# Optimization experiments

Measured on AMD Instinct MI355X. Metric: run time of the kernel, lower is better.

The kernel has to match this reference:

```python
import jax, jax.numpy as jnp
import numpy as np

B, L = 4096, 200
N_USERS, N_ITEMS, N_CATS, N_DUR = 200000, 500000, 1000, 20
D = 64  # item_embed_dim == seq_embed_dim


def _lin(k, din, dout):
    kw, kb = jax.random.split(k)
    s = 1.0 / np.sqrt(din)
    return (jax.random.uniform(kw, (din, dout), minval=-s, maxval=s),
            jax.random.uniform(kb, (dout,), minval=-s, maxval=s))


def setup_inputs() -> dict:
    key = jax.random.key(0)
    ks = jax.random.split(key, 20)
    inp = {
        'user_id': jax.random.randint(ks[0], (B,), 0, N_USERS),
        'item_id': jax.random.randint(ks[1], (B,), 0, N_ITEMS),
        'item_category': jax.random.randint(ks[2], (B,), 0, N_CATS),
        'item_dur_bkt': jax.random.randint(ks[3], (B,), 0, N_DUR),
        'user_dense': jax.random.normal(ks[4], (B, 25), dtype=jnp.float32),
        'item_dense': jax.random.normal(ks[5], (B, 3), dtype=jnp.float32),
        'history_seq': jax.random.randint(ks[6], (B, L), 0, N_ITEMS + 1),
        # embedding tables (init std=0.01 as in _init_weights)
        'user_W': 0.01 * jax.random.normal(ks[7], (N_USERS, 64), dtype=jnp.float32),
        'item_W': 0.01 * jax.random.normal(ks[8], (N_ITEMS, D), dtype=jnp.float32),
        'cat_W': 0.01 * jax.random.normal(ks[9], (N_CATS, 16), dtype=jnp.float32),
        'dur_W': 0.01 * jax.random.normal(ks[10], (N_DUR, 8), dtype=jnp.float32),
        'hist_W': 0.01 * jax.random.normal(ks[11], (N_ITEMS + 1, D), dtype=jnp.float32),
    }
    # attention MLP: 4*D=256 -> 64 -> 32 -> 1
    inp['aW0'], inp['ab0'] = _lin(ks[12], 4 * D, 64)
    inp['aW1'], inp['ab1'] = _lin(ks[13], 64, 32)
    inp['aW2'], inp['ab2'] = _lin(ks[14], 32, 1)
    # final MLP: concat_dim 64+64+16+8+25+3+64 = 244 -> 256 -> 128 -> 1
    inp['mW0'], inp['mb0'] = _lin(ks[15], 244, 256)
    inp['mW1'], inp['mb1'] = _lin(ks[16], 256, 128)
    inp['mW2'], inp['mb2'] = _lin(ks[17], 128, 1)
    return inp


def reference(user_id, item_id, item_category, item_dur_bkt, user_dense, item_dense,
              history_seq, user_W, item_W, cat_W, dur_W, hist_W,
              aW0, ab0, aW1, ab1, aW2, ab2, mW0, mb0, mW1, mb1, mW2, mb2):
    u_emb = user_W[user_id]            # (B, 64)
    i_emb = item_W[item_id]            # (B, D)
    c_emb = cat_W[item_category]       # (B, 16)
    d_emb = dur_W[item_dur_bkt]        # (B, 8)
    hist = hist_W[history_seq]         # (B, L, D)

    t = i_emb[:, None, :]              # (B, 1, D); item_dim == seq_dim so no slice
    tb = jnp.broadcast_to(t, hist.shape)
    feat = jnp.concatenate([hist, tb, hist * t, hist - t], axis=-1)  # (B, L, 4D)

    h = jax.nn.relu(feat @ aW0 + ab0)
    h = jax.nn.relu(h @ aW1 + ab1)
    scores = (h @ aW2 + ab2)[..., 0]   # (B, L)

    pad_mask = history_seq == 0
    scores = jnp.where(pad_mask, jnp.float32(-1e9), scores)
    w = jax.nn.softmax(scores, axis=-1)                # (B, L)
    pooled = jnp.einsum('bl,bld->bd', w, hist)         # (B, D)

    x = jnp.concatenate([u_emb, i_emb, c_emb, d_emb, user_dense, item_dense, pooled], axis=-1)
    h = jax.nn.relu(x @ mW0 + mb0)     # dropout is identity in eval mode
    h = jax.nn.relu(h @ mW1 + mb1)
    logit = (h @ mW2 + mb2)[..., 0]
    return jax.nn.sigmoid(logit)       # (B,)
```

## Files before the change

kernel.cpp:

```cpp
#include <hip/hip_runtime.h>

#define L_SZ 200
#define RB 8
#define HS_STRIDE 72

typedef __attribute__((ext_vector_type(8))) short short8;
typedef __attribute__((ext_vector_type(4))) float floatx4;

__device__ __forceinline__ unsigned short f2bf(float f) {
    unsigned int u = __float_as_uint(f);
    unsigned int r = (u + 0x7fffu + ((u >> 16) & 1u)) >> 16;
    return (unsigned short)r;
}
__device__ __forceinline__ float bf2f(unsigned short h) {
    return __uint_as_float(((unsigned int)h) << 16);
}
__device__ __forceinline__ float wave_sum64(float v) {
    #pragma unroll
    for (int m = 1; m <= 32; m <<= 1) v += __shfl_xor(v, m, 64);
    return v;
}
__device__ __forceinline__ float wave_max64(float v) {
    #pragma unroll
    for (int m = 1; m <= 32; m <<= 1) v = fmaxf(v, __shfl_xor(v, m, 64));
    return v;
}
__device__ __forceinline__ unsigned int pk2(float a, float b) {
    return ((unsigned int)f2bf(b) << 16) | (unsigned int)f2bf(a);
}

__global__ __launch_bounds__(256) void prep_kernel(
    const int* __restrict__ item_id, const float* __restrict__ item_W,
    const float* __restrict__ aW0, const float* __restrict__ ab0,
    const float* __restrict__ aW1,
    float* __restrict__ T1t, float* __restrict__ T2t,
    unsigned short* __restrict__ PW1, float* __restrict__ cb_ws)
{
    __shared__ float shbuf[3 * 64 * 65];
    const int tid = threadIdx.x;
    if (blockIdx.x == 0) {
        #pragma unroll
        for (int t = 0; t < 3; ++t) {
            const int r0 = (t == 0) ? 0 : (t == 1) ? 128 : 192;
            for (int u = tid; u < 1024; u += 256) {
                int k = u >> 4, c4 = u & 15;
                float4 v = *(const float4*)(aW0 + (r0 + k) * 64 + c4 * 4);
                float* dst = shbuf + t * 4160 + k * 65 + c4 * 4;
                dst[0] = v.x; dst[1] = v.y; dst[2] = v.z; dst[3] = v.w;
            }
        }
        __syncthreads();
        for (int u = tid; u < 4096; u += 256) {
            int j = u >> 6, k = u & 63;
            T1t[u] = shbuf[k * 65 + j] + shbuf[2 * 4160 + k * 65 + j];
            T2t[u] = shbuf[4160 + k * 65 + j];
        }
        for (int u = tid; u < 2048; u += 256) {
            int i = u & 7, lane = (u >> 3) & 63, f = u >> 9;
            int nt = f >> 1, ks = f & 1;
            int k = ks * 32 + (lane >> 4) * 8 + i;
            int n = nt * 16 + (lane & 15);
            PW1[u] = f2bf(aW1[k * 32 + n]);
        }
    } else {
        for (int u = tid; u < 4096; u += 256) {
            int k = u >> 6, j = u & 63;
            shbuf[k * 65 + j] = aW0[(64 + k) * 64 + j] - aW0[(192 + k) * 64 + j];
        }
        __syncthreads();
        const int bl = tid >> 6, j = tid & 63;
        const int b = (blockIdx.x - 1) * 4 + bl;
        const float* ie = item_W + (size_t)item_id[b] * 64;
        float acc = ab0[j];
        #pragma unroll 8
        for (int k = 0; k < 64; ++k) acc = fmaf(ie[k], shbuf[k * 65 + j], acc);
        cb_ws[(size_t)b * 64 + j] = acc;
    }
}

__global__ __launch_bounds__(256, 4) void attn_kernel(
    const int* __restrict__ item_id, const int* __restrict__ hist_seq,
    const float* __restrict__ item_W, const float* __restrict__ hist_W,
    const float* __restrict__ T1t, const float* __restrict__ T2t,
    const unsigned short* __restrict__ PW1, const float* __restrict__ cb_ws,
    const float* __restrict__ ab1, const float* __restrict__ aW2,
    const float* __restrict__ ab2, float* __restrict__ pooled_ws)
{
    __shared__ __align__(16) unsigned char smem[38624];
    unsigned short* Hs  = (unsigned short*)(smem);
    unsigned short* BB  = (unsigned short*)(smem + 28800);
    int*   seq_sh = (int*)(smem + 36992);
    float* scores = (float*)(smem + 37792);
    float* red    = (float*)(smem + 38592);

    const int tid  = threadIdx.x;
    const int w    = tid >> 6;
    const int lane = tid & 63;
    const int b    = blockIdx.x;
    const int* hseq = hist_seq + b * L_SZ;

    if (tid < L_SZ) seq_sh[tid] = hseq[tid];

    const int rbase = tid >> 3, c8 = tid & 7;
    const bool extra = tid < 64;
    const int r6 = extra ? 192 + rbase : 0;
    const float* sp[7];
    #pragma unroll
    for (int t = 0; t < 6; ++t)
        sp[t] = hist_W + (size_t)hseq[rbase + t * 32] * 64 + c8 * 8;
    sp[6] = hist_W + (size_t)hseq[r6] * 64 + c8 * 8;
    float4 f0[7], f1[7];
    #pragma unroll
    for (int t = 0; t < 7; ++t) {
        f0[t] = *(const float4*)sp[t];
        f1[t] = *(const float4*)(sp[t] + 4);
    }

    const int c = lane & 15, q = lane >> 4;
    short8 bW1[2][2];
    #pragma unroll
    for (int nt = 0; nt < 2; ++nt)
        #pragma unroll
        for (int ks = 0; ks < 2; ++ks)
            bW1[nt][ks] = *(const short8*)(PW1 + ((nt * 2 + ks) * 64 + lane) * 8);
    float cbr[4];
    #pragma unroll
    for (int nt = 0; nt < 4; ++nt) cbr[nt] = cb_ws[(size_t)b * 64 + nt * 16 + c];
    float ab1r[2], aw2r[2];
    #pragma unroll
    for (int nt = 0; nt < 2; ++nt) {
        ab1r[nt] = ab1[nt * 16 + c];
        aw2r[nt] = aW2[nt * 16 + c];
    }
    const float ab2s = ab2[0];

    #pragma unroll
    for (int t = 0; t < 6; ++t) {
        uint4 pk;
        pk.x = pk2(f0[t].x, f0[t].y); pk.y = pk2(f0[t].z, f0[t].w);
        pk.z = pk2(f1[t].x, f1[t].y); pk.w = pk2(f1[t].z, f1[t].w);
        *(uint4*)(Hs + (rbase + t * 32) * HS_STRIDE + c8 * 8) = pk;
    }
    if (extra) {
        uint4 pk;
        pk.x = pk2(f0[6].x, f0[6].y); pk.y = pk2(f0[6].z, f0[6].w);
        pk.z = pk2(f1[6].x, f1[6].y); pk.w = pk2(f1[6].z, f1[6].w);
        *(uint4*)(Hs + r6 * HS_STRIDE + c8 * 8) = pk;
    }

    {
        const float* irow = item_W + (size_t)item_id[b] * 64;
        const int j0 = tid >> 3;
        float4 em0 = *(const float4*)(irow + c8 * 8);
        float4 em1 = *(const float4*)(irow + c8 * 8 + 4);
        #pragma unroll
        for (int t = 0; t < 2; ++t) {
            int j = j0 + t * 32;
            const float* p1 = T1t + j * 64 + c8 * 8;
            const float* p2 = T2t + j * 64 + c8 * 8;
            float4 a0 = *(const float4*)p1, a1 = *(const float4*)(p1 + 4);
            float4 b0 = *(const float4*)p2, b1 = *(const float4*)(p2 + 4);
            float v[8];
            v[0] = a0.x + em0.x * b0.x; v[1] = a0.y + em0.y * b0.y;
            v[2] = a0.z + em0.z * b0.z; v[3] = a0.w + em0.w * b0.w;
            v[4] = a1.x + em1.x * b1.x; v[5] = a1.y + em1.y * b1.y;
            v[6] = a1.z + em1.z * b1.z; v[7] = a1.w + em1.w * b1.w;
            uint4 pk;
            pk.x = pk2(v[0], v[1]); pk.y = pk2(v[2], v[3]);
            pk.z = pk2(v[4], v[5]); pk.w = pk2(v[6], v[7]);
            *(uint4*)(BB + j * 64 + (c8 ^ (j & 7)) * 8) = pk;
        }
    }
    __syncthreads();

    short8 bW[4][2];
    #pragma unroll
    for (int nt = 0; nt < 4; ++nt)
        #pragma unroll
        for (int ks = 0; ks < 2; ++ks)
            bW[nt][ks] = *(const short8*)(BB + (nt * 16 + c) * 64
                                             + ((4 * ks + q) ^ (c & 7)) * 8);
    __syncthreads();

    unsigned short* scrw = BB + w * (16 * 64);
    const floatx4 zf = {0.f, 0.f, 0.f, 0.f};

    for (int mt = w; mt < 13; mt += 4) {
        const int rowbase = mt * 16;
        floatx4 acc0[4] = {zf, zf, zf, zf};
        #pragma unroll
        for (int ks = 0; ks < 2; ++ks) {
            short8 a = *(const short8*)(Hs + (rowbase + c) * HS_STRIDE + ks * 32 + q * 8);
            acc0[0] = __builtin_amdgcn_mfma_f32_16x16x32_bf16(a, bW[0][ks], acc0[0], 0, 0, 0);
            acc0[1] = __builtin_amdgcn_mfma_f32_16x16x32_bf16(a, bW[1][ks], acc0[1], 0, 0, 0);
            acc0[2] = __builtin_amdgcn_mfma_f32_16x16x32_bf16(a, bW[2][ks], acc0[2], 0, 0, 0);
            acc0[3] = __builtin_amdgcn_mfma_f32_16x16x32_bf16(a, bW[3][ks], acc0[3], 0, 0, 0);
        }
        #pragma unroll
        for (int nt = 0; nt < 4; ++nt)
            #pragma unroll
            for (int r = 0; r < 4; ++r) {
                float h = fmaxf(acc0[nt][r] + cbr[nt], 0.f);
                int row = q * 4 + r;
                int gp = (2 * nt + (c >> 3)) ^ (row & 7);
                scrw[row * 64 + gp * 8 + (c & 7)] = f2bf(h);
            }
        floatx4 acc1[2] = {zf, zf};
        #pragma unroll
        for (int ks = 0; ks < 2; ++ks) {
            short8 a1 = *(const short8*)(scrw + c * 64 + ((4 * ks + q) ^ (c & 7)) * 8);
            acc1[0] = __builtin_amdgcn_mfma_f32_16x16x32_bf16(a1, bW1[0][ks], acc1[0], 0, 0, 0);
            acc1[1] = __builtin_amdgcn_mfma_f32_16x16x32_bf16(a1, bW1[1][ks], acc1[1], 0, 0, 0);
        }
        float s[4];
        #pragma unroll
        for (int r = 0; r < 4; ++r)
            s[r] = fmaxf(acc1[0][r] + ab1r[0], 0.f) * aw2r[0]
                 + fmaxf(acc1[1][r] + ab1r[1], 0.f) * aw2r[1];
        #pragma unroll
        for (int m = 1; m <= 8; m <<= 1)
            #pragma unroll
            for (int r = 0; r < 4; ++r) s[r] += __shfl_xor(s[r], m, 64);
        if (c == 0) {
            #pragma unroll
            for (int r = 0; r < 4; ++r) {
                int l = rowbase + q * 4 + r;
                if (l < L_SZ)
                    scores[l] = (seq_sh[l] == 0) ? -1.0e9f : (s[r] + ab2s);
            }
        }
    }
    __syncthreads();

    float s0 = (tid < L_SZ) ? scores[tid] : -3.0e38f;
    float mx = wave_max64(s0);
    if (lane == 0) red[w] = mx;
    __syncthreads();
    mx = fmaxf(fmaxf(red[0], red[1]), fmaxf(red[2], red[3]));
    float e = (tid < L_SZ) ? __expf(s0 - mx) : 0.f;
    float sm = wave_sum64(e);
    if (lane == 0) red[4 + w] = sm;
    __syncthreads();
    const float winv = 1.f / ((red[4] + red[5]) + (red[6] + red[7]));
    if (tid < L_SZ) scores[tid] = e * winv;
    __syncthreads();

    float* pools = (float*)BB;
    {
        int g  = (w << 1) | (lane >> 5);
        int jj = lane & 31;
        int l0 = g * 26, l1 = (l0 + 26 < L_SZ) ? l0 + 26 : L_SZ;
        float p0 = 0.f, p1 = 0.f;
        for (int l = l0; l < l1; ++l) {
            float wt = scores[l];
            unsigned int pv = *(const unsigned int*)(Hs + l * HS_STRIDE + jj * 2);
            p0 = fmaf(wt, bf2f((unsigned short)(pv & 0xffffu)), p0);
            p1 = fmaf(wt, bf2f((unsigned short)(pv >> 16)), p1);
        }
        float2 pp = {p0, p1};
        *(float2*)&pools[g * 64 + jj * 2] = pp;
    }
    __syncthreads();
    if (tid < 64) {
        float sum = 0.f;
        #pragma unroll
        for (int g = 0; g < 8; ++g) sum += pools[g * 64 + tid];
        pooled_ws[(size_t)b * 64 + tid] = sum;
    }
}

__global__ __launch_bounds__(256) void mlp_kernel(
    const int* __restrict__ user_id, const int* __restrict__ item_id,
    const int* __restrict__ item_cat, const int* __restrict__ item_dur,
    const float* __restrict__ user_dense, const float* __restrict__ item_dense,
    const float* __restrict__ user_W, const float* __restrict__ item_W,
    const float* __restrict__ cat_W, const float* __restrict__ dur_W,
    const float* __restrict__ mW0, const float* __restrict__ mb0,
    const float* __restrict__ mW1, const float* __restrict__ mb1,
    const float* __restrict__ mW2, const float* __restrict__ mb2,
    const float* __restrict__ pooled_ws, float* __restrict__ out)
{
    __shared__ __align__(16) float xT[244][RB];
    __shared__ __align__(16) float h0T[256][RB];
    __shared__ __align__(16) float h1T[128][RB];
    __shared__ __align__(16) float part[128][RB];

    const int tid = threadIdx.x;
    const int b0 = blockIdx.x * RB;

    for (int idx = tid; idx < 244 * RB; idx += 256) {
        int r = idx / 244;
        int c = idx - r * 244;
        int b = b0 + r;
        float v;
        if (c < 64)       v = user_W[(size_t)user_id[b] * 64 + c];
        else if (c < 128) v = item_W[(size_t)item_id[b] * 64 + (c - 64)];
        else if (c < 144) v = cat_W[item_cat[b] * 16 + (c - 128)];
        else if (c < 152) v = dur_W[item_dur[b] * 8 + (c - 144)];
        else if (c < 177) v = user_dense[b * 25 + (c - 152)];
        else if (c < 180) v = item_dense[b * 3 + (c - 177)];
        else              v = pooled_ws[(size_t)b * 64 + (c - 180)];
        xT[c][r] = v;
    }
    __syncthreads();

    {
        float acc[RB];
        const float bias = mb0[tid];
        #pragma unroll
        for (int r = 0; r < RB; ++r) acc[r] = bias;
        #pragma unroll 4
        for (int k = 0; k < 244; ++k) {
            float wk = mW0[k * 256 + tid];
            float4 xa = *(const float4*)&xT[k][0];
            float4 xb = *(const float4*)&xT[k][4];
            acc[0] = fmaf(wk, xa.x, acc[0]);
            acc[1] = fmaf(wk, xa.y, acc[1]);
            acc[2] = fmaf(wk, xa.z, acc[2]);
            acc[3] = fmaf(wk, xa.w, acc[3]);
            acc[4] = fmaf(wk, xb.x, acc[4]);
            acc[5] = fmaf(wk, xb.y, acc[5]);
            acc[6] = fmaf(wk, xb.z, acc[6]);
            acc[7] = fmaf(wk, xb.w, acc[7]);
        }
        #pragma unroll
        for (int r = 0; r < RB; ++r) h0T[tid][r] = fmaxf(acc[r], 0.f);
    }
    __syncthreads();

    const int jj = tid & 127;
    const int half = tid >> 7;
    {
        float acc[RB];
        #pragma unroll
        for (int r = 0; r < RB; ++r) acc[r] = 0.f;
        #pragma unroll 4
        for (int t = 0; t < 128; ++t) {
            int k = half * 128 + t;
            float wk = mW1[k * 128 + jj];
            float4 ha = *(const float4*)&h0T[k][0];
            float4 hb = *(const float4*)&h0T[k][4];
            acc[0] = fmaf(wk, ha.x, acc[0]);
            acc[1] = fmaf(wk, ha.y, acc[1]);
            acc[2] = fmaf(wk, ha.z, acc[2]);
            acc[3] = fmaf(wk, ha.w, acc[3]);
            acc[4] = fmaf(wk, hb.x, acc[4]);
            acc[5] = fmaf(wk, hb.y, acc[5]);
            acc[6] = fmaf(wk, hb.z, acc[6]);
            acc[7] = fmaf(wk, hb.w, acc[7]);
        }
        if (half == 1) {
            #pragma unroll
            for (int r = 0; r < RB; ++r) part[jj][r] = acc[r];
        }
        __syncthreads();
        if (half == 0) {
            const float bias = mb1[jj];
            #pragma unroll
            for (int r = 0; r < RB; ++r)
                h1T[jj][r] = fmaxf(acc[r] + part[jj][r] + bias, 0.f);
        }
    }
    __syncthreads();

    if (tid < RB) {
        const int r = tid;
        float a0 = mb2[0], a1 = 0.f;
        #pragma unroll 8
        for (int k = 0; k < 128; k += 2) {
            a0 = fmaf(h1T[k][r],     mW2[k],     a0);
            a1 = fmaf(h1T[k + 1][r], mW2[k + 1], a1);
        }
        float a = a0 + a1;
        out[b0 + r] = 1.f / (1.f + __expf(-a));
    }
}

extern "C" void kernel_launch(void* const* d_in, const int* in_sizes, int n_in,
                              void* d_out, int out_size, void* d_ws, size_t ws_size,
                              hipStream_t stream) {
    (void)in_sizes; (void)n_in; (void)out_size; (void)ws_size;
    const int*   user_id    = (const int*)d_in[0];
    const int*   item_id    = (const int*)d_in[1];
    const int*   item_cat   = (const int*)d_in[2];
    const int*   item_dur   = (const int*)d_in[3];
    const float* user_dense = (const float*)d_in[4];
    const float* item_dense = (const float*)d_in[5];
    const int*   hist_seq   = (const int*)d_in[6];
    const float* user_W     = (const float*)d_in[7];
    const float* item_W     = (const float*)d_in[8];
    const float* cat_W      = (const float*)d_in[9];
    const float* dur_W      = (const float*)d_in[10];
    const float* hist_W     = (const float*)d_in[11];
    const float* aW0 = (const float*)d_in[12];
    const float* ab0 = (const float*)d_in[13];
    const float* aW1 = (const float*)d_in[14];
    const float* ab1 = (const float*)d_in[15];
    const float* aW2 = (const float*)d_in[16];
    const float* ab2 = (const float*)d_in[17];
    const float* mW0 = (const float*)d_in[18];
    const float* mb0 = (const float*)d_in[19];
    const float* mW1 = (const float*)d_in[20];
    const float* mb1 = (const float*)d_in[21];
    const float* mW2 = (const float*)d_in[22];
    const float* mb2 = (const float*)d_in[23];
    float* out = (float*)d_out;

    char* ws = (char*)d_ws;
    float* pooled_ws = (float*)ws;
    float* cb_ws     = (float*)(ws + (1u << 20));
    float* T1t       = (float*)(ws + (2u << 20));
    float* T2t       = (float*)(ws + (2u << 20) + 16384);
    unsigned short* PW1 = (unsigned short*)(ws + (2u << 20) + 32768);

    prep_kernel<<<1025, 256, 0, stream>>>(item_id, item_W, aW0, ab0, aW1,
                                          T1t, T2t, PW1, cb_ws);
    attn_kernel<<<4096, 256, 0, stream>>>(item_id, hist_seq, item_W, hist_W,
                                          T1t, T2t, PW1, cb_ws,
                                          ab1, aW2, ab2, pooled_ws);
    mlp_kernel<<<4096 / RB, 256, 0, stream>>>(user_id, item_id, item_cat, item_dur,
                                              user_dense, item_dense,
                                              user_W, item_W, cat_W, dur_W,
                                              mW0, mb0, mW1, mb1, mW2, mb2,
                                              pooled_ws, out);
}
```

Baseline: 388.7 us.

## Process four batch rows per attention block with prefetched history gathers

The attention kernel now handles four batch elements per block in a loop. It prefetches the next element's sequence indices and history embedding rows into registers while the current element's MFMA scoring, softmax and pooling run, using double-buffered sequence arrays. __syncthreads is replaced by an explicit lgkmcnt wait plus barrier, and the prep kernel now handles 64 rows per block with the projection matrix loaded once into shared memory. The aim is to hide gather latency and amortise per-block setup, at the cost of fewer blocks (1024) and higher register pressure from the prefetch buffers.

```diff
diff --git a/kernel.cpp b/kernel.cpp
--- a/kernel.cpp
+++ b/kernel.cpp
@@ -2,6 +2,7 @@
 
 #define L_SZ 200
 #define RB 8
+#define ELEMS 4
 #define HS_STRIDE 72
 
 typedef __attribute__((ext_vector_type(8))) short short8;
@@ -27,6 +28,11 @@
 }
 __device__ __forceinline__ unsigned int pk2(float a, float b) {
     return ((unsigned int)f2bf(b) << 16) | (unsigned int)f2bf(a);
+}
+__device__ __forceinline__ void bar_lds() {
+    asm volatile("s_waitcnt lgkmcnt(0)" ::: "memory");
+    __builtin_amdgcn_s_barrier();
+    asm volatile("" ::: "memory");
 }
 
 __global__ __launch_bounds__(256) void prep_kernel(
@@ -63,18 +69,27 @@
             PW1[u] = f2bf(aW1[k * 32 + n]);
         }
     } else {
+        float* T3 = shbuf;
+        float* IE = shbuf + 64 * 65;
+        const int B0 = (blockIdx.x - 1) * 64;
         for (int u = tid; u < 4096; u += 256) {
             int k = u >> 6, j = u & 63;
-            shbuf[k * 65 + j] = aW0[(64 + k) * 64 + j] - aW0[(192 + k) * 64 + j];
+            T3[k * 65 + j] = aW0[(64 + k) * 64 + j] - aW0[(192 + k) * 64 + j];
+        }
+        for (int u = tid; u < 4096; u += 256) {
+            int r = u >> 6, j = u & 63;
+            IE[r * 64 + j] = item_W[(size_t)item_id[B0 + r] * 64 + j];
         }
         __syncthreads();
-        const int bl = tid >> 6, j = tid & 63;
-        const int b = (blockIdx.x - 1) * 4 + bl;
-        const float* ie = item_W + (size_t)item_id[b] * 64;
-        float acc = ab0[j];
-        #pragma unroll 8
-        for (int k = 0; k < 64; ++k) acc = fmaf(ie[k], shbuf[k * 65 + j], acc);
-        cb_ws[(size_t)b * 64 + j] = acc;
+        const int j = tid & 63, rg = tid >> 6;
+        for (int pass = 0; pass < 16; ++pass) {
+            int bl = rg * 16 + pass;
+            float acc = ab0[j];
+            #pragma unroll 8
+            for (int k = 0; k < 64; ++k)
+                acc = fmaf(IE[bl * 64 + k], T3[k * 65 + j], acc);
+            cb_ws[(size_t)(B0 + bl) * 64 + j] = acc;
+        }
     }
 }
 
@@ -86,46 +101,28 @@
     const float* __restrict__ ab1, const float* __restrict__ aW2,
     const float* __restrict__ ab2, float* __restrict__ pooled_ws)
 {
-    __shared__ __align__(16) unsigned char smem[38624];
+    __shared__ __align__(16) unsigned char smem[39424];
     unsigned short* Hs  = (unsigned short*)(smem);
     unsigned short* BB  = (unsigned short*)(smem + 28800);
-    int*   seq_sh = (int*)(smem + 36992);
-    float* scores = (float*)(smem + 37792);
-    float* red    = (float*)(smem + 38592);
+    int*   seqA   = (int*)(smem + 36992);
+    int*   seqB   = (int*)(smem + 37792);
+    float* scores = (float*)(smem + 38592);
+    float* red    = (float*)(smem + 39392);
 
     const int tid  = threadIdx.x;
     const int w    = tid >> 6;
     const int lane = tid & 63;
-    const int b    = blockIdx.x;
-    const int* hseq = hist_seq + b * L_SZ;
-
-    if (tid < L_SZ) seq_sh[tid] = hseq[tid];
-
+    const int c = lane & 15, q = lane >> 4;
     const int rbase = tid >> 3, c8 = tid & 7;
     const bool extra = tid < 64;
-    const int r6 = extra ? 192 + rbase : 0;
-    const float* sp[7];
-    #pragma unroll
-    for (int t = 0; t < 6; ++t)
-        sp[t] = hist_W + (size_t)hseq[rbase + t * 32] * 64 + c8 * 8;
-    sp[6] = hist_W + (size_t)hseq[r6] * 64 + c8 * 8;
-    float4 f0[7], f1[7];
-    #pragma unroll
-    for (int t = 0; t < 7; ++t) {
-        f0[t] = *(const float4*)sp[t];
-        f1[t] = *(const float4*)(sp[t] + 4);
-    }
-
-    const int c = lane & 15, q = lane >> 4;
+    const int b0 = blockIdx.x * ELEMS;
+
     short8 bW1[2][2];
     #pragma unroll
     for (int nt = 0; nt < 2; ++nt)
         #pragma unroll
         for (int ks = 0; ks < 2; ++ks)
             bW1[nt][ks] = *(const short8*)(PW1 + ((nt * 2 + ks) * 64 + lane) * 8);
-    float cbr[4];
-    #pragma unroll
-    for (int nt = 0; nt < 4; ++nt) cbr[nt] = cb_ws[(size_t)b * 64 + nt * 16 + c];
     float ab1r[2], aw2r[2];
     #pragma unroll
     for (int nt = 0; nt < 2; ++nt) {
@@ -133,139 +130,192 @@
         aw2r[nt] = aW2[nt * 16 + c];
     }
     const float ab2s = ab2[0];
-
-    #pragma unroll
-    for (int t = 0; t < 6; ++t) {
-        uint4 pk;
-        pk.x = pk2(f0[t].x, f0[t].y); pk.y = pk2(f0[t].z, f0[t].w);
-        pk.z = pk2(f1[t].x, f1[t].y); pk.w = pk2(f1[t].z, f1[t].w);
-        *(uint4*)(Hs + (rbase + t * 32) * HS_STRIDE + c8 * 8) = pk;
-    }
-    if (extra) {
-        uint4 pk;
-        pk.x = pk2(f0[6].x, f0[6].y); pk.y = pk2(f0[6].z, f0[6].w);
-        pk.z = pk2(f1[6].x, f1[6].y); pk.w = pk2(f1[6].z, f1[6].w);
-        *(uint4*)(Hs + r6 * HS_STRIDE + c8 * 8) = pk;
-    }
-
+    int iid[ELEMS];
+    #pragma unroll
+    for (int e = 0; e < ELEMS; ++e) iid[e] = item_id[b0 + e];
+
+    int* seq_cur = seqA;
+    int* seq_nxt = seqB;
+    int si[7];
     {
-        const float* irow = item_W + (size_t)item_id[b] * 64;
-        const int j0 = tid >> 3;
-        float4 em0 = *(const float4*)(irow + c8 * 8);
-        float4 em1 = *(const float4*)(irow + c8 * 8 + 4);
-        #pragma unroll
-        for (int t = 0; t < 2; ++t) {
-            int j = j0 + t * 32;
-            const float* p1 = T1t + j * 64 + c8 * 8;
-            const float* p2 = T2t + j * 64 + c8 * 8;
-            float4 a0 = *(const float4*)p1, a1 = *(const float4*)(p1 + 4);
-            float4 b0 = *(const float4*)p2, b1 = *(const float4*)(p2 + 4);
-            float v[8];
-            v[0] = a0.x + em0.x * b0.x; v[1] = a0.y + em0.y * b0.y;
-            v[2] = a0.z + em0.z * b0.z; v[3] = a0.w + em0.w * b0.w;
-            v[4] = a1.x + em1.x * b1.x; v[5] = a1.y + em1.y * b1.y;
-            v[6] = a1.z + em1.z * b1.z; v[7] = a1.w + em1.w * b1.w;
+        const int* hq = hist_seq + (size_t)b0 * L_SZ;
+        #pragma unroll
+        for (int t = 0; t < 6; ++t) si[t] = hq[rbase + t * 32];
+        si[6] = hq[extra ? 192 + rbase : 0];
+    }
+    #pragma unroll
+    for (int t = 0; t < 6; ++t) seq_cur[rbase + t * 32] = si[t];
+    if (extra) seq_cur[192 + rbase] = si[6];
+    float4 f0[7], f1[7];
+    #pragma unroll
+    for (int t = 0; t < 7; ++t) {
+        const float* p = hist_W + (size_t)si[t] * 64 + c8 * 8;
+        f0[t] = *(const float4*)p;
+        f1[t] = *(const float4*)(p + 4);
+    }
+
+    #pragma unroll 1
+    for (int e = 0; e < ELEMS; ++e) {
+        const int b = b0 + e;
+        if (e + 1 < ELEMS) {
+            const int* hq = hist_seq + (size_t)(b + 1) * L_SZ;
+            #pragma unroll
+            for (int t = 0; t < 6; ++t) si[t] = hq[rbase + t * 32];
+            si[6] = hq[extra ? 192 + rbase : 0];
+        }
+        float cbr[4];
+        #pragma unroll
+        for (int nt = 0; nt < 4; ++nt)
+            cbr[nt] = cb_ws[(size_t)b * 64 + nt * 16 + c];
+
+        #pragma unroll
+        for (int t = 0; t < 6; ++t) {
             uint4 pk;
-            pk.x = pk2(v[0], v[1]); pk.y = pk2(v[2], v[3]);
-            pk.z = pk2(v[4], v[5]); pk.w = pk2(v[6], v[7]);
-            *(uint4*)(BB + j * 64 + (c8 ^ (j & 7)) * 8) = pk;
-        }
-    }
-    __syncthreads();
-
-    short8 bW[4][2];
-    #pragma unroll
-    for (int nt = 0; nt < 4; ++nt)
-        #pragma unroll
-        for (int ks = 0; ks < 2; ++ks)
-            bW[nt][ks] = *(const short8*)(BB + (nt * 16 + c) * 64
-                                             + ((4 * ks + q) ^ (c & 7)) * 8);
-    __syncthreads();
-
-    unsigned short* scrw = BB + w * (16 * 64);
-    const floatx4 zf = {0.f, 0.f, 0.f, 0.f};
-
-    for (int mt = w; mt < 13; mt += 4) {
-        const int rowbase = mt * 16;
-        floatx4 acc0[4] = {zf, zf, zf, zf};
-        #pragma unroll
-        for (int ks = 0; ks < 2; ++ks) {
-            short8 a = *(const short8*)(Hs + (rowbase + c) * HS_STRIDE + ks * 32 + q * 8);
-            acc0[0] = __builtin_amdgcn_mfma_f32_16x16x32_bf16(a, bW[0][ks], acc0[0], 0, 0, 0);
-            acc0[1] = __builtin_amdgcn_mfma_f32_16x16x32_bf16(a, bW[1][ks], acc0[1], 0, 0, 0);
-            acc0[2] = __builtin_amdgcn_mfma_f32_16x16x32_bf16(a, bW[2][ks], acc0[2], 0, 0, 0);
-            acc0[3] = __builtin_amdgcn_mfma_f32_16x16x32_bf16(a, bW[3][ks], acc0[3], 0, 0, 0);
-        }
+            pk.x = pk2(f0[t].x, f0[t].y); pk.y = pk2(f0[t].z, f0[t].w);
+            pk.z = pk2(f1[t].x, f1[t].y); pk.w = pk2(f1[t].z, f1[t].w);
+            *(uint4*)(Hs + (rbase + t * 32) * HS_STRIDE + c8 * 8) = pk;
+        }
+        if (extra) {
+            uint4 pk;
+            pk.x = pk2(f0[6].x, f0[6].y); pk.y = pk2(f0[6].z, f0[6].w);
+            pk.z = pk2(f1[6].x, f1[6].y); pk.w = pk2(f1[6].z, f1[6].w);
+            *(uint4*)(Hs + (192 + rbase) * HS_STRIDE + c8 * 8) = pk;
+        }
+
+        {
+            const float* irow = item_W + (size_t)iid[e] * 64;
+            const int j0 = tid >> 3;
+            float4 em0 = *(const float4*)(irow + c8 * 8);
+            float4 em1 = *(const float4*)(irow + c8 * 8 + 4);
+            #pragma unroll
+            for (int t = 0; t < 2; ++t) {
+                int j = j0 + t * 32;
+                const float* p1 = T1t + j * 64 + c8 * 8;
+                const float* p2 = T2t + j * 64 + c8 * 8;
+                float4 a0 = *(const float4*)p1, a1 = *(const float4*)(p1 + 4);
+                float4 b0v = *(const float4*)p2, b1v = *(const float4*)(p2 + 4);
+                float v[8];
+                v[0] = a0.x + em0.x * b0v.x; v[1] = a0.y + em0.y * b0v.y;
+                v[2] = a0.z + em0.z * b0v.z; v[3] = a0.w + em0.w * b0v.w;
+                v[4] = a1.x + em1.x * b1v.x; v[5] = a1.y + em1.y * b1v.y;
+                v[6] = a1.z + em1.z * b1v.z; v[7] = a1.w + em1.w * b1v.w;
+                uint4 pk;
+                pk.x = pk2(v[0], v[1]); pk.y = pk2(v[2], v[3]);
+                pk.z = pk2(v[4], v[5]); pk.w = pk2(v[6], v[7]);
+                *(uint4*)(BB + j * 64 + (c8 ^ (j & 7)) * 8) = pk;
+            }
+        }
+        bar_lds();
+
+        short8 bW[4][2];
         #pragma unroll
         for (int nt = 0; nt < 4; ++nt)
             #pragma unroll
-            for (int r = 0; r < 4; ++r) {
-                float h = fmaxf(acc0[nt][r] + cbr[nt], 0.f);
-                int row = q * 4 + r;
-                int gp = (2 * nt + (c >> 3)) ^ (row & 7);
-                scrw[row * 64 + gp * 8 + (c & 7)] = f2bf(h);
-            }
-        floatx4 acc1[2] = {zf, zf};
-        #pragma unroll
-        for (int ks = 0; ks < 2; ++ks) {
-            short8 a1 = *(const short8*)(scrw + c * 64 + ((4 * ks + q) ^ (c & 7)) * 8);
-            acc1[0] = __builtin_amdgcn_mfma_f32_16x16x32_bf16(a1, bW1[0][ks], acc1[0], 0, 0, 0);
-            acc1[1] = __builtin_amdgcn_mfma_f32_16x16x32_bf16(a1, bW1[1][ks], acc1[1], 0, 0, 0);
-        }
-        float s[4];
-        #pragma unroll
-        for (int r = 0; r < 4; ++r)
-            s[r] = fmaxf(acc1[0][r] + ab1r[0], 0.f) * aw2r[0]
-                 + fmaxf(acc1[1][r] + ab1r[1], 0.f) * aw2r[1];
-        #pragma unroll
-        for (int m = 1; m <= 8; m <<= 1)
-            #pragma unroll
-            for (int r = 0; r < 4; ++r) s[r] += __shfl_xor(s[r], m, 64);
-        if (c == 0) {
-            #pragma unroll
-            for (int r = 0; r < 4; ++r) {
-                int l = rowbase + q * 4 + r;
-                if (l < L_SZ)
-                    scores[l] = (seq_sh[l] == 0) ? -1.0e9f : (s[r] + ab2s);
-            }
-        }
-    }
-    __syncthreads();
-
-    float s0 = (tid < L_SZ) ? scores[tid] : -3.0e38f;
-    float mx = wave_max64(s0);
-    if (lane == 0) red[w] = mx;
-    __syncthreads();
-    mx = fmaxf(fmaxf(red[0], red[1]), fmaxf(red[2], red[3]));
-    float e = (tid < L_SZ) ? __expf(s0 - mx) : 0.f;
-    float sm = wave_sum64(e);
-    if (lane == 0) red[4 + w] = sm;
-    __syncthreads();
-    const float winv = 1.f / ((red[4] + red[5]) + (red[6] + red[7]));
-    if (tid < L_SZ) scores[tid] = e * winv;
-    __syncthreads();
-
-    float* pools = (float*)BB;
-    {
-        int g  = (w << 1) | (lane >> 5);
-        int jj = lane & 31;
-        int l0 = g * 26, l1 = (l0 + 26 < L_SZ) ? l0 + 26 : L_SZ;
-        float p0 = 0.f, p1 = 0.f;
-        for (int l = l0; l < l1; ++l) {
-            float wt = scores[l];
-            unsigned int pv = *(const unsigned int*)(Hs + l * HS_STRIDE + jj * 2);
-            p0 = fmaf(wt, bf2f((unsigned short)(pv & 0xffffu)), p0);
-            p1 = fmaf(wt, bf2f((unsigned short)(pv >> 16)), p1);
-        }
-        float2 pp = {p0, p1};
-        *(float2*)&pools[g * 64 + jj * 2] = pp;
-    }
-    __syncthreads();
-    if (tid < 64) {
-        float sum = 0.f;
-        #pragma unroll
-        for (int g = 0; g < 8; ++g) sum += pools[g * 64 + tid];
-        pooled_ws[(size_t)b * 64 + tid] = sum;
+            for (int ks = 0; ks < 2; ++ks)
+                bW[nt][ks] = *(const short8*)(BB + (nt * 16 + c) * 64
+                                                 + ((4 * ks + q) ^ (c & 7)) * 8);
+        bar_lds();
+
+        if (e + 1 < ELEMS) {
+            #pragma unroll
+            for (int t = 0; t < 6; ++t) seq_nxt[rbase + t * 32] = si[t];
+            if (extra) seq_nxt[192 + rbase] = si[6];
+            #pragma unroll
+            for (int t = 0; t < 7; ++t) {
+                const float* p = hist_W + (size_t)si[t] * 64 + c8 * 8;
+                f0[t] = *(const float4*)p;
+                f1[t] = *(const float4*)(p + 4);
+            }
+        }
+
+        unsigned short* scrw = BB + w * (16 * 64);
+        const floatx4 zf = {0.f, 0.f, 0.f, 0.f};
+
+        for (int mt = w; mt < 13; mt += 4) {
+            const int rowbase = mt * 16;
+            floatx4 acc0[4] = {zf, zf, zf, zf};
+            #pragma unroll
+            for (int ks = 0; ks < 2; ++ks) {
+                short8 a = *(const short8*)(Hs + (rowbase + c) * HS_STRIDE + ks * 32 + q * 8);
+                acc0[0] = __builtin_amdgcn_mfma_f32_16x16x32_bf16(a, bW[0][ks], acc0[0], 0, 0, 0);
+                acc0[1] = __builtin_amdgcn_mfma_f32_16x16x32_bf16(a, bW[1][ks], acc0[1], 0, 0, 0);
+                acc0[2] = __builtin_amdgcn_mfma_f32_16x16x32_bf16(a, bW[2][ks], acc0[2], 0, 0, 0);
+                acc0[3] = __builtin_amdgcn_mfma_f32_16x16x32_bf16(a, bW[3][ks], acc0[3], 0, 0, 0);
+            }
+            #pragma unroll
+            for (int nt = 0; nt < 4; ++nt)
+                #pragma unroll
+                for (int r = 0; r < 4; ++r) {
+                    float h = fmaxf(acc0[nt][r] + cbr[nt], 0.f);
+                    int row = q * 4 + r;
+                    int gp = (2 * nt + (c >> 3)) ^ (row & 7);
+                    scrw[row * 64 + gp * 8 + (c & 7)] = f2bf(h);
+                }
+            floatx4 acc1[2] = {zf, zf};
+            #pragma unroll
+            for (int ks = 0; ks < 2; ++ks) {
+                short8 a1 = *(const short8*)(scrw + c * 64 + ((4 * ks + q) ^ (c & 7)) * 8);
+                acc1[0] = __builtin_amdgcn_mfma_f32_16x16x32_bf16(a1, bW1[0][ks], acc1[0], 0, 0, 0);
+                acc1[1] = __builtin_amdgcn_mfma_f32_16x16x32_bf16(a1, bW1[1][ks], acc1[1], 0, 0, 0);
+            }
+            float s[4];
+            #pragma unroll
+            for (int r = 0; r < 4; ++r)
+                s[r] = fmaxf(acc1[0][r] + ab1r[0], 0.f) * aw2r[0]
+                     + fmaxf(acc1[1][r] + ab1r[1], 0.f) * aw2r[1];
+            #pragma unroll
+            for (int m = 1; m <= 8; m <<= 1)
+                #pragma unroll
+                for (int r = 0; r < 4; ++r) s[r] += __shfl_xor(s[r], m, 64);
+            if (c == 0) {
+                #pragma unroll
+                for (int r = 0; r < 4; ++r) {
+                    int l = rowbase + q * 4 + r;
+                    if (l < L_SZ)
+                        scores[l] = (seq_cur[l] == 0) ? -1.0e9f : (s[r] + ab2s);
+                }
+            }
+        }
+        bar_lds();
+
+        float s0 = (tid < L_SZ) ? scores[tid] : -3.0e38f;
+        float mx = wave_max64(s0);
+        if (lane == 0) red[w] = mx;
+        bar_lds();
+        mx = fmaxf(fmaxf(red[0], red[1]), fmaxf(red[2], red[3]));
+        float ev = (tid < L_SZ) ? __expf(s0 - mx) : 0.f;
+        float sm = wave_sum64(ev);
+        if (lane == 0) red[4 + w] = sm;
+        bar_lds();
+        const float winv = 1.f / ((red[4] + red[5]) + (red[6] + red[7]));
+        if (tid < L_SZ) scores[tid] = ev * winv;
+        bar_lds();
+
+        float* pools = (float*)BB;
+        {
+            int g  = (w << 1) | (lane >> 5);
+            int jj = lane & 31;
+            int l0 = g * 26, l1 = (l0 + 26 < L_SZ) ? l0 + 26 : L_SZ;
+            float p0 = 0.f, p1 = 0.f;
+            for (int l = l0; l < l1; ++l) {
+                float wt = scores[l];
+                unsigned int pv = *(const unsigned int*)(Hs + l * HS_STRIDE + jj * 2);
+                p0 = fmaf(wt, bf2f((unsigned short)(pv & 0xffffu)), p0);
+                p1 = fmaf(wt, bf2f((unsigned short)(pv >> 16)), p1);
+            }
+            float2 pp = {p0, p1};
+            *(float2*)&pools[g * 64 + jj * 2] = pp;
+        }
+        bar_lds();
+        if (tid < 64) {
+            float sum = 0.f;
+            #pragma unroll
+            for (int g = 0; g < 8; ++g) sum += pools[g * 64 + tid];
+            pooled_ws[(size_t)b * 64 + tid] = sum;
+        }
+        bar_lds();
+
+        int* tp = seq_cur; seq_cur = seq_nxt; seq_nxt = tp;
     }
 }
 
@@ -413,11 +463,11 @@
     float* T2t       = (float*)(ws + (2u << 20) + 16384);
     unsigned short* PW1 = (unsigned short*)(ws + (2u << 20) + 32768);
 
-    prep_kernel<<<1025, 256, 0, stream>>>(item_id, item_W, aW0, ab0, aW1,
-                                          T1t, T2t, PW1, cb_ws);
-    attn_kernel<<<4096, 256, 0, stream>>>(item_id, hist_seq, item_W, hist_W,
-                                          T1t, T2t, PW1, cb_ws,
-                                          ab1, aW2, ab2, pooled_ws);
+    prep_kernel<<<65, 256, 0, stream>>>(item_id, item_W, aW0, ab0, aW1,
+                                        T1t, T2t, PW1, cb_ws);
+    attn_kernel<<<4096 / ELEMS, 256, 0, stream>>>(item_id, hist_seq, item_W, hist_W,
+                                                  T1t, T2t, PW1, cb_ws,
+                                                  ab1, aW2, ab2, pooled_ws);
     mlp_kernel<<<4096 / RB, 256, 0, stream>>>(user_id, item_id, item_cat, item_dur,
                                               user_dense, item_dense,
                                               user_W, item_W, cat_W, dur_W,
```

Result: slower. 532.1 us (+36.9%).
